# Performance work log

Hardware: AMD Instinct MI355X
Metric: run time of the kernel (lower is better)

## Reference

```python
import jax, jax.numpy as jnp
import numpy as np

B, C, F_IN, F_OUT, K, NCLS = 2048, 62, 512, 256, 5, 2
THRESH = 0.1  # adjacency threshold from source


def setup_inputs() -> dict:
    key = jax.random.key(0)
    ks = jax.random.split(key, 12)
    n = lambda k, shape, s=1.0: jax.random.normal(k, shape, jnp.float32) * s
    return {
        "x": n(ks[0], (B, C, F_IN)),
        "coord": n(ks[1], (C, C, 4), 0.2),
        "adj_w1": n(ks[2], (4, 64), 0.5),
        "adj_b1": n(ks[3], (64,), 0.1),
        "adj_w2": n(ks[4], (64, 1), 0.3),
        "adj_b2": n(ks[5], (1,), 0.1),
        "cheb_W": n(ks[6], (K, F_IN, F_OUT), 0.04),
        "cheb_b": n(ks[7], (F_OUT,), 0.02),
        "conv_w": n(ks[8], (1, 1, 1, 1), 1.0),
        "conv_b": n(ks[9], (1,), 0.1),
        "fc_w": n(ks[10], (C * F_OUT, NCLS), 0.01),
        "fc_b": n(ks[11], (NCLS,), 0.0),
    }


def reference(x, coord, adj_w1, adj_b1, adj_w2, adj_b2, cheb_W, cheb_b,
              conv_w, conv_b, fc_w, fc_b):
    # --- learned adjacency W_star = adj_fc(coord).squeeze() ---
    h = jax.nn.relu(coord @ adj_w1 + adj_b1)          # [C, C, 64]
    W_star = (h @ adj_w2 + adj_b2)[..., 0]            # [C, C]
    Cn = W_star.shape[0]
    eye = jnp.eye(Cn, dtype=bool)
    # thresholded edges; get_laplacian removes self-loops first
    A = jnp.where((W_star > THRESH) & ~eye, W_star, 0.0)
    # sym-normalized scaled Laplacian with lambda_max=2 (PyG ChebConv default):
    # L_hat = 2*(I - D^-1/2 A D^-1/2)/2 - I = -D^-1/2 A D^-1/2 (zero diagonal)
    deg = A.sum(axis=1)                               # row sums (source nodes)
    safe = jnp.where(deg > 0, deg, 1.0)
    dis = jnp.where(deg > 0, jax.lax.rsqrt(safe), 0.0)
    L = -(dis[:, None] * A * dis[None, :])            # [C, C]

    # --- Chebyshev recursion: Tx0 = x, Tx1 = L x, Tx_k = 2 L Tx_{k-1} - Tx_{k-2} ---
    Tx0 = x                                           # [B, C, F_in]
    out = Tx0 @ cheb_W[0]                             # [B, C, F_out]
    Tx1 = jnp.einsum('ij,bjf->bif', L, Tx0)
    out = out + Tx1 @ cheb_W[1]
    for k in range(2, cheb_W.shape[0]):
        Tx2 = 2.0 * jnp.einsum('ij,bjf->bif', L, Tx1) - Tx0
        out = out + Tx2 @ cheb_W[k]
        Tx0, Tx1 = Tx1, Tx2
    out = out + cheb_b

    # --- 1x1 Conv2d with 1 in/out channel == scalar affine ---
    out = conv_w[0, 0, 0, 0] * out + conv_b[0]
    # --- flatten + FC head ---
    return out.reshape(out.shape[0], -1) @ fc_w + fc_b  # [B, n_classes]
```

## Files before the change

### kernel.cpp

```cpp
#include <hip/hip_runtime.h>

#define CN   62
#define FIN  512
#define FOUT 256
#define KCH  5
#define JF   (CN*FIN)
#define JF4  (JF/4)
#define CC   (CN*CN)

typedef float v4 __attribute__((ext_vector_type(4)));
typedef float v2 __attribute__((ext_vector_type(2)));

__global__ __launch_bounds__(512) void k_pre(
    const float* __restrict__ coord, const float* __restrict__ w1,
    const float* __restrict__ b1, const float* __restrict__ w2,
    const float* __restrict__ b2, const float* __restrict__ chebW,
    const float* __restrict__ fcw, float* __restrict__ Pg,
    float* __restrict__ S2)
{
    __shared__ float smem[24128];
    const int tid = threadIdx.x;
    const int bid = blockIdx.x;

    if (bid == 0) {
        float* sL  = smem;
        float* sB0 = smem + 3844;
        float* sB1 = smem + 7688;
        float* sB2 = smem + 11532;
        float* sDis= smem + 15376;

        for (int e = tid; e < CC; e += 512) {
            int i = e / CN, j = e % CN;
            float c0 = coord[e*4+0], c1 = coord[e*4+1];
            float c2 = coord[e*4+2], c3 = coord[e*4+3];
            float acc = b2[0];
            for (int u = 0; u < 64; ++u) {
                float h = b1[u] + c0*w1[u] + c1*w1[64+u] + c2*w1[128+u] + c3*w1[192+u];
                acc += fmaxf(h, 0.0f) * w2[u];
            }
            sL[e] = (acc > 0.1f && i != j) ? acc : 0.0f;
        }
        __syncthreads();

        if (tid < CN) {
            float d = 0.f;
            for (int j = 0; j < CN; ++j) d += sL[tid*CN + j];
            sDis[tid] = (d > 0.f) ? (1.0f / sqrtf(d)) : 0.f;
        }
        __syncthreads();

        for (int e = tid; e < CC; e += 512) {
            int i = e / CN, j = e % CN;
            float l = -(sDis[i] * sL[e] * sDis[j]);
            sL[e]  = l;
            float id = (i == j) ? 1.f : 0.f;
            sB0[e] = id;
            sB1[e] = l;
            Pg[e]      = id;
            Pg[CC + e] = l;
        }
        __syncthreads();

        float* bufs[3] = { sB0, sB1, sB2 };
        for (int k = 2; k < KCH; ++k) {
            float* Pa = bufs[(k-2) % 3];
            float* Pb = bufs[(k-1) % 3];
            float* Pc = bufs[k % 3];
            for (int e = tid; e < CC; e += 512) {
                int i = e / CN, j = e % CN;
                float s = 0.f;
                for (int m = 0; m < CN; ++m) s += sL[i*CN + m] * Pb[m*CN + j];
                float v = 2.f * s - Pa[e];
                Pc[e] = v;
                Pg[k*CC + e] = v;
            }
            __syncthreads();
        }
    } else {
        int b  = bid - 1;
        int k  = b >> 5;
        int r  = b & 31;
        int f0 = (r >> 1) * 32;
        int ch = r & 1;

        float* sW = smem;
        float* sF = smem + 8256;

        const float* cwb = chebW + (size_t)(k*FIN + f0) * FOUT;
        for (int i = tid; i < 32*256; i += 512) {
            int rr = i >> 8, q = i & 255;
            sW[rr*258 + q] = cwb[rr*256 + q];
        }
        const float* fb = fcw + (size_t)(ch*31) * 512;
        for (int i = tid; i < 31*512; i += 512) {
            sF[i] = fb[i];
        }
        __syncthreads();

        int f_local = tid & 31;
        int c_local = tid >> 5;
        const float* wrow = sW + f_local*258;

        #pragma unroll
        for (int pass = 0; pass < 2; ++pass) {
            int c_l = c_local + pass*16;
            if (c_l >= 31) break;
            const v2* frow = (const v2*)(sF + c_l*512);
            float a0 = 0.f, a1 = 0.f;
            #pragma unroll 4
            for (int fo = 0; fo < 256; ++fo) {
                float w = wrow[fo];
                v2 fv = frow[fo];
                a0 += w * fv.x;
                a1 += w * fv.y;
            }
            size_t base = ((size_t)((k*62 + ch*31 + c_l)*2))*512 + f0 + f_local;
            S2[base]       = a0;
            S2[base + 512] = a1;
        }
    }
}

__global__ __launch_bounds__(256) void k_G3(
    const float* __restrict__ Pg, const float* __restrict__ S2,
    const float* __restrict__ chebb, const float* __restrict__ convw,
    const float* __restrict__ convb, const float* __restrict__ fcw,
    const float* __restrict__ fcb, float* __restrict__ G,
    float* __restrict__ constv)
{
    const int tid = threadIdx.x;
    const int bid = blockIdx.x;
    __shared__ float sP[310];
    __shared__ float sp4[4];

    if (bid < 124) {
        int n = bid / CN, j = bid % CN;
        for (int i = tid; i < 310; i += 256) {
            int k = i / CN, c = i % CN;
            sP[i] = Pg[k*CC + c*CN + j];
        }
        __syncthreads();

        const v2* s2 = (const v2*)S2;
        float a0 = 0.f, a1 = 0.f;
        #pragma unroll 5
        for (int i = 0; i < 310; ++i) {
            float p = sP[i];
            v2 v = s2[(size_t)(i*2 + n)*256 + tid];
            a0 += p * v.x;
            a1 += p * v.y;
        }
        float cw = convw[0];
        v2 res; res.x = cw*a0; res.y = cw*a1;
        ((v2*)(G + (size_t)n*JF + j*512))[tid] = res;
    } else {
        int w = tid >> 6, lane = tid & 63;
        int n = w & 1, half = w >> 1;
        float cw = convw[0], cb = convb[0];
        float acc = 0.f;
        for (int idx = lane + 64*half; idx < CN*FOUT; idx += 128) {
            int fo = idx & 255;
            acc += (cw * chebb[fo] + cb) * fcw[idx*2 + n];
        }
        for (int o = 32; o > 0; o >>= 1) acc += __shfl_down(acc, o, 64);
        if (lane == 0) sp4[w] = acc;
        __syncthreads();
        if (tid < 2) constv[tid] = sp4[tid] + sp4[tid + 2] + fcb[tid];
    }
}

__global__ __launch_bounds__(256) void k_main(
    const float* __restrict__ x, const float* __restrict__ G,
    const float* __restrict__ constv, float* __restrict__ out)
{
    const int tid = threadIdx.x;
    const int b0  = blockIdx.x * 4;
    const v4* g0 = (const v4*)(G);
    const v4* g1 = (const v4*)(G + JF);
    const v4* x0 = (const v4*)(x + (size_t)b0 * JF);

    float a00=0, a01=0, a10=0, a11=0, a20=0, a21=0, a30=0, a31=0;

    #pragma unroll 2
    for (int i = tid; i < JF4; i += 256) {
        v4 gg0 = g0[i];
        v4 gg1 = g1[i];
        v4 x0v = __builtin_nontemporal_load(&x0[i]);
        v4 x1v = __builtin_nontemporal_load(&x0[JF4 + i]);
        v4 x2v = __builtin_nontemporal_load(&x0[2*JF4 + i]);
        v4 x3v = __builtin_nontemporal_load(&x0[3*JF4 + i]);
        a00 += x0v.x*gg0.x + x0v.y*gg0.y + x0v.z*gg0.z + x0v.w*gg0.w;
        a01 += x0v.x*gg1.x + x0v.y*gg1.y + x0v.z*gg1.z + x0v.w*gg1.w;
        a10 += x1v.x*gg0.x + x1v.y*gg0.y + x1v.z*gg0.z + x1v.w*gg0.w;
        a11 += x1v.x*gg1.x + x1v.y*gg1.y + x1v.z*gg1.z + x1v.w*gg1.w;
        a20 += x2v.x*gg0.x + x2v.y*gg0.y + x2v.z*gg0.z + x2v.w*gg0.w;
        a21 += x2v.x*gg1.x + x2v.y*gg1.y + x2v.z*gg1.z + x2v.w*gg1.w;
        a30 += x3v.x*gg0.x + x3v.y*gg0.y + x3v.z*gg0.z + x3v.w*gg0.w;
        a31 += x3v.x*gg1.x + x3v.y*gg1.y + x3v.z*gg1.z + x3v.w*gg1.w;
    }

    float vals[8] = { a00, a01, a10, a11, a20, a21, a30, a31 };
    for (int o = 32; o > 0; o >>= 1) {
        #pragma unroll
        for (int q = 0; q < 8; ++q) vals[q] += __shfl_down(vals[q], o, 64);
    }

    __shared__ float sred[4][8];
    int wave = tid >> 6, lane = tid & 63;
    if (lane == 0) {
        #pragma unroll
        for (int q = 0; q < 8; ++q) sred[wave][q] = vals[q];
    }
    __syncthreads();
    if (tid < 8) {
        float s = sred[0][tid] + sred[1][tid] + sred[2][tid] + sred[3][tid];
        int r = tid >> 1, n = tid & 1;
        out[(b0 + r)*2 + n] = s + constv[n];
    }
}

extern "C" void kernel_launch(void* const* d_in, const int* in_sizes, int n_in,
                              void* d_out, int out_size, void* d_ws, size_t ws_size,
                              hipStream_t stream)
{
    const float* x     = (const float*)d_in[0];
    const float* coord = (const float*)d_in[1];
    const float* aw1   = (const float*)d_in[2];
    const float* ab1   = (const float*)d_in[3];
    const float* aw2   = (const float*)d_in[4];
    const float* ab2   = (const float*)d_in[5];
    const float* chebW = (const float*)d_in[6];
    const float* chebb = (const float*)d_in[7];
    const float* convw = (const float*)d_in[8];
    const float* convb = (const float*)d_in[9];
    const float* fcw   = (const float*)d_in[10];
    const float* fcb   = (const float*)d_in[11];
    float* out = (float*)d_out;

    float* ws = (float*)d_ws;
    float* Pg = ws;
    float* S2 = Pg + KCH*CC;
    float* G  = S2 + KCH*CN*2*FIN;
    float* cv = G + 2*JF;

    k_pre <<<161, 512, 0, stream>>>(coord, aw1, ab1, aw2, ab2, chebW, fcw, Pg, S2);
    k_G3  <<<125, 256, 0, stream>>>(Pg, S2, chebb, convw, convb, fcw, fcb, G, cv);
    k_main<<<512, 256, 0, stream>>>(x, G, cv, out);
}
```

Measured before the change: 423.5 us.

## Register-tile Chebyshev polynomial matmul and vectorize S2 projection in k_pre

Block 0's Chebyshev polynomial powers now use a padded 64-wide shared layout. Each thread keeps one row of L in registers and computes eight output columns with v4 LDS loads, replacing the scalar per-element dot products. The S2 blocks use a 260-float pitch and v4 loads, and handle both channel passes in a single fused loop. This targets the serial latency of the single-block polynomial chain in the precompute kernel, at the cost of more registers and some padding logic. The main x-streaming kernel, which likely dominates the runtime, is unchanged.

```diff
diff --git a/kernel.cpp b/kernel.cpp
--- a/kernel.cpp
+++ b/kernel.cpp
@@ -1,12 +1,14 @@
 #include <hip/hip_runtime.h>
 
 #define CN   62
+#define CNP  64
 #define FIN  512
 #define FOUT 256
 #define KCH  5
 #define JF   (CN*FIN)
 #define JF4  (JF/4)
 #define CC   (CN*CN)
+#define WPAD 260
 
 typedef float v4 __attribute__((ext_vector_type(4)));
 typedef float v2 __attribute__((ext_vector_type(2)));
@@ -18,16 +20,16 @@
     const float* __restrict__ fcw, float* __restrict__ Pg,
     float* __restrict__ S2)
 {
-    __shared__ float smem[24128];
+    __shared__ float smem[24704];
     const int tid = threadIdx.x;
     const int bid = blockIdx.x;
 
     if (bid == 0) {
         float* sL  = smem;
-        float* sB0 = smem + 3844;
-        float* sB1 = smem + 7688;
-        float* sB2 = smem + 11532;
-        float* sDis= smem + 15376;
+        float* sB0 = smem + 3968;
+        float* sB1 = smem + 7936;
+        float* sB2 = smem + 11904;
+        float* sDis= smem + 15872;
 
         for (int e = tid; e < CC; e += 512) {
             int i = e / CN, j = e % CN;
@@ -38,44 +40,80 @@
                 float h = b1[u] + c0*w1[u] + c1*w1[64+u] + c2*w1[128+u] + c3*w1[192+u];
                 acc += fmaxf(h, 0.0f) * w2[u];
             }
-            sL[e] = (acc > 0.1f && i != j) ? acc : 0.0f;
+            sL[i*CNP + j] = (acc > 0.1f && i != j) ? acc : 0.0f;
+        }
+        for (int z = tid; z < 4*128; z += 512) {
+            smem[(z >> 7)*3968 + 62*CNP + (z & 127)] = 0.f;
+        }
+        if (tid < 4*62) {
+            int b = tid / CN, rr = tid % CN;
+            float* p = smem + b*3968 + rr*CNP;
+            p[62] = 0.f; p[63] = 0.f;
         }
         __syncthreads();
 
         if (tid < CN) {
             float d = 0.f;
-            for (int j = 0; j < CN; ++j) d += sL[tid*CN + j];
+            for (int jj = 0; jj < CN; ++jj) {
+                int j = jj + tid; if (j >= CN) j -= CN;
+                d += sL[tid*CNP + j];
+            }
             sDis[tid] = (d > 0.f) ? (1.0f / sqrtf(d)) : 0.f;
         }
         __syncthreads();
 
         for (int e = tid; e < CC; e += 512) {
             int i = e / CN, j = e % CN;
-            float l = -(sDis[i] * sL[e] * sDis[j]);
-            sL[e]  = l;
+            float l = -(sDis[i] * sL[i*CNP + j] * sDis[j]);
+            sL[i*CNP + j] = l;
             float id = (i == j) ? 1.f : 0.f;
-            sB0[e] = id;
-            sB1[e] = l;
+            sB0[i*CNP + j] = id;
+            sB1[i*CNP + j] = l;
             Pg[e]      = id;
             Pg[CC + e] = l;
         }
         __syncthreads();
 
-        float* bufs[3] = { sB0, sB1, sB2 };
-        for (int k = 2; k < KCH; ++k) {
-            float* Pa = bufs[(k-2) % 3];
-            float* Pb = bufs[(k-1) % 3];
-            float* Pc = bufs[k % 3];
-            for (int e = tid; e < CC; e += 512) {
-                int i = e / CN, j = e % CN;
-                float s = 0.f;
-                for (int m = 0; m < CN; ++m) s += sL[i*CN + m] * Pb[m*CN + j];
-                float v = 2.f * s - Pa[e];
-                Pc[e] = v;
-                Pg[k*CC + e] = v;
+        const int i  = tid >> 3;
+        const int j0 = (tid & 7) * 8;
+        float Lr[CNP];
+        if (i < CN) {
+            #pragma unroll
+            for (int m4 = 0; m4 < 16; ++m4) {
+                v4 t = *(const v4*)(sL + i*CNP + m4*4);
+                Lr[m4*4+0] = t.x; Lr[m4*4+1] = t.y;
+                Lr[m4*4+2] = t.z; Lr[m4*4+3] = t.w;
+            }
+        }
+
+        auto cheb_step = [&](const float* Pa, const float* Pb, float* Pc, int k) {
+            if (i < CN) {
+                v4 acc0 = {0.f,0.f,0.f,0.f}, acc1 = {0.f,0.f,0.f,0.f};
+                #pragma unroll
+                for (int m = 0; m < CNP; ++m) {
+                    float lm = Lr[m];
+                    v4 p0 = *(const v4*)(Pb + m*CNP + j0);
+                    v4 p1 = *(const v4*)(Pb + m*CNP + j0 + 4);
+                    acc0 += lm * p0;
+                    acc1 += lm * p1;
+                }
+                v4 pa0 = *(const v4*)(Pa + i*CNP + j0);
+                v4 pa1 = *(const v4*)(Pa + i*CNP + j0 + 4);
+                v4 r0 = 2.f*acc0 - pa0;
+                v4 r1 = 2.f*acc1 - pa1;
+                *(v4*)(Pc + i*CNP + j0)     = r0;
+                *(v4*)(Pc + i*CNP + j0 + 4) = r1;
+                float ov[8] = {r0.x,r0.y,r0.z,r0.w,r1.x,r1.y,r1.z,r1.w};
+                float* pgk = Pg + (size_t)k*CC + i*CN + j0;
+                #pragma unroll
+                for (int t = 0; t < 8; ++t)
+                    if (j0 + t < CN) pgk[t] = ov[t];
             }
             __syncthreads();
-        }
+        };
+        cheb_step(sB0, sB1, sB2, 2);
+        cheb_step(sB1, sB2, sB0, 3);
+        cheb_step(sB2, sB0, sB1, 4);
     } else {
         int b  = bid - 1;
         int k  = b >> 5;
@@ -84,39 +122,43 @@
         int ch = r & 1;
 
         float* sW = smem;
-        float* sF = smem + 8256;
+        float* sF = smem + 8320;
 
         const float* cwb = chebW + (size_t)(k*FIN + f0) * FOUT;
-        for (int i = tid; i < 32*256; i += 512) {
-            int rr = i >> 8, q = i & 255;
-            sW[rr*258 + q] = cwb[rr*256 + q];
+        for (int idx = tid; idx < 32*256; idx += 512) {
+            int rr = idx >> 8, q = idx & 255;
+            sW[rr*WPAD + q] = cwb[rr*256 + q];
         }
         const float* fb = fcw + (size_t)(ch*31) * 512;
-        for (int i = tid; i < 31*512; i += 512) {
-            sF[i] = fb[i];
-        }
-        __syncthreads();
-
-        int f_local = tid & 31;
-        int c_local = tid >> 5;
-        const float* wrow = sW + f_local*258;
-
-        #pragma unroll
-        for (int pass = 0; pass < 2; ++pass) {
-            int c_l = c_local + pass*16;
-            if (c_l >= 31) break;
-            const v2* frow = (const v2*)(sF + c_l*512);
-            float a0 = 0.f, a1 = 0.f;
-            #pragma unroll 4
-            for (int fo = 0; fo < 256; ++fo) {
-                float w = wrow[fo];
-                v2 fv = frow[fo];
-                a0 += w * fv.x;
-                a1 += w * fv.y;
-            }
-            size_t base = ((size_t)((k*62 + ch*31 + c_l)*2))*512 + f0 + f_local;
-            S2[base]       = a0;
-            S2[base + 512] = a1;
+        for (int idx = tid; idx < 31*512; idx += 512) sF[idx] = fb[idx];
+        __syncthreads();
+
+        const int f_local = tid & 31;
+        const int c_local = tid >> 5;
+        const int c0 = c_local;
+        const int c1 = (c_local < 15) ? (c_local + 16) : 15;
+        const v4* wr4   = (const v4*)(sW + f_local*WPAD);
+        const v4* frow0 = (const v4*)(sF + c0*512);
+        const v4* frow1 = (const v4*)(sF + c1*512);
+
+        float a00 = 0.f, a01 = 0.f, a10 = 0.f, a11 = 0.f;
+        #pragma unroll 4
+        for (int q = 0; q < 64; ++q) {
+            v4 w4  = wr4[q];
+            v4 f00 = frow0[2*q], f01 = frow0[2*q + 1];
+            v4 f10 = frow1[2*q], f11 = frow1[2*q + 1];
+            a00 += w4.x*f00.x + w4.y*f00.z + w4.z*f01.x + w4.w*f01.z;
+            a01 += w4.x*f00.y + w4.y*f00.w + w4.z*f01.y + w4.w*f01.w;
+            a10 += w4.x*f10.x + w4.y*f10.z + w4.z*f11.x + w4.w*f11.z;
+            a11 += w4.x*f10.y + w4.y*f10.w + w4.z*f11.y + w4.w*f11.w;
+        }
+        size_t base0 = ((size_t)((k*62 + ch*31 + c0)*2))*512 + f0 + f_local;
+        S2[base0]       = a00;
+        S2[base0 + 512] = a01;
+        if (c_local < 15) {
+            size_t base1 = ((size_t)((k*62 + ch*31 + c_local + 16)*2))*512 + f0 + f_local;
+            S2[base1]       = a10;
+            S2[base1 + 512] = a11;
         }
     }
 }
```

Result: faster. 404.9 us (-4.4%).
